# Optimization experiments

Measured on AMD Instinct MI355X. Metric: run time of the kernel, lower is better.

The kernel has to match this reference:

```python
import jax, jax.numpy as jnp
import numpy as np

B, T, IN = 32, 1024, 256
H = 128          # hidden_size
NL = 2           # num_layers
NC = 4           # num_classes
F2 = 2 * H       # bidirectional feature size


def _lstm_dir(xs, w_ih, w_hh, b_ih, b_hh, reverse):
    # xs: [T, B, in]; w_ih: [4H, in]; w_hh: [4H, H]
    if reverse:
        xs = xs[::-1]
    h0 = jnp.zeros((xs.shape[1], H), xs.dtype)
    c0 = jnp.zeros((xs.shape[1], H), xs.dtype)

    def step(carry, xt):
        h, c = carry
        g = xt @ w_ih.T + b_ih + h @ w_hh.T + b_hh  # [B, 4H]
        i, f, gg, o = jnp.split(g, 4, axis=-1)       # PyTorch gate order i,f,g,o
        c = jax.nn.sigmoid(f) * c + jax.nn.sigmoid(i) * jnp.tanh(gg)
        h = jax.nn.sigmoid(o) * jnp.tanh(c)
        return (h, c), h

    _, hs = jax.lax.scan(step, (h0, c0), xs)  # [T, B, H]
    if reverse:
        hs = hs[::-1]
    return hs


def setup_inputs() -> dict:
    key = jax.random.key(0)
    ks = jax.random.split(key, 12)
    s = 0.05
    x = jax.random.normal(ks[0], (B, T, IN), jnp.float32)
    # stacked LSTM params: [layer, direction, ...]; layer0 in = IN, layer1 in = 2H = IN
    w_ih = jax.random.normal(ks[1], (NL, 2, 4 * H, IN), jnp.float32) * s
    w_hh = jax.random.normal(ks[2], (NL, 2, 4 * H, H), jnp.float32) * s
    b_ih = jax.random.normal(ks[3], (NL, 2, 4 * H), jnp.float32) * s
    b_hh = jax.random.normal(ks[4], (NL, 2, 4 * H), jnp.float32) * s
    wq = jax.random.normal(ks[5], (F2, F2), jnp.float32) * s
    wk = jax.random.normal(ks[6], (F2, F2), jnp.float32) * s
    wv = jax.random.normal(ks[7], (F2, F2), jnp.float32) * s
    bq = jax.random.normal(ks[8], (F2,), jnp.float32) * s
    bk = jax.random.normal(ks[9], (F2,), jnp.float32) * s
    bv = jax.random.normal(ks[10], (F2,), jnp.float32) * s
    w_fc = jax.random.normal(ks[11], (NC, F2), jnp.float32) * s
    b_fc = jnp.zeros((NC,), jnp.float32)
    return {"x": x, "w_ih": w_ih, "w_hh": w_hh, "b_ih": b_ih, "b_hh": b_hh,
            "wq": wq, "wk": wk, "wv": wv, "bq": bq, "bk": bk, "bv": bv,
            "w_fc": w_fc, "b_fc": b_fc}


def reference(x, w_ih, w_hh, b_ih, b_hh, wq, wk, wv, bq, bk, bv, w_fc, b_fc):
    # --- biLSTM (eval mode: inter-layer dropout inactive) ---
    xs = jnp.swapaxes(x, 0, 1)  # time-major [T, B, IN]
    for l in range(NL):
        fwd = _lstm_dir(xs, w_ih[l, 0], w_hh[l, 0], b_ih[l, 0], b_hh[l, 0], False)
        bwd = _lstm_dir(xs, w_ih[l, 1], w_hh[l, 1], b_ih[l, 1], b_hh[l, 1], True)
        xs = jnp.concatenate([fwd, bwd], axis=-1)  # [T, B, 2H]
    out = jnp.swapaxes(xs, 0, 1)  # [B, T, 2H]
    # --- naive full self-attention ---
    q = out @ wq.T + bq
    k = out @ wk.T + bk
    v = out @ wv.T + bv
    scores = jnp.einsum('btd,bsd->bts', q, k) / jnp.sqrt(jnp.float32(F2))
    attn = jax.nn.softmax(scores, axis=-1)          # [B, T, T]
    ctx = jnp.einsum('bts,bsd->btd', attn, v)       # [B, T, 2H]
    # --- FC head on last timestep ---
    return ctx[:, -1, :] @ w_fc.T + b_fc            # [B, NC]
```

## Files before the change

kernel.cpp:

```cpp
#include <hip/hip_runtime.h>
#include <math.h>
#include <stdint.h>

#define BB 32
#define TT 1024
#define HH 128
#define G4 512
#define CH 16
#define XPS 516

typedef _Float16 half2_t __attribute__((ext_vector_type(2)));
typedef _Float16 half8_t __attribute__((ext_vector_type(8)));
typedef float f32x4 __attribute__((ext_vector_type(4)));

__device__ __forceinline__ float fdot2f(half2_t a, half2_t b, float c) {
    return __builtin_amdgcn_fdot2(a, b, c, false);
}
__device__ __forceinline__ float rcpf(float x) {
    return __builtin_amdgcn_rcpf(x);
}
__device__ __forceinline__ float dpp_xor1(float x) {
    return __builtin_bit_cast(float, __builtin_amdgcn_update_dpp(
        0, __builtin_bit_cast(int, x), 0xB1, 0xF, 0xF, true));
}
__device__ __forceinline__ float dpp_xor2(float x) {
    return __builtin_bit_cast(float, __builtin_amdgcn_update_dpp(
        0, __builtin_bit_cast(int, x), 0x4E, 0xF, 0xF, true));
}
__device__ __forceinline__ void bar_lgkm() {
    asm volatile("s_waitcnt lgkmcnt(0)\n\ts_barrier" ::: "memory");
}

__global__ __launch_bounds__(256) void cvt_wih(
    const float* __restrict__ w, _Float16* __restrict__ o,
    float* __restrict__ ctxw, float* __restrict__ den, int* __restrict__ cnt)
{
    const int i = (blockIdx.x * 256 + threadIdx.x) * 4;
    float4 f = *(const float4*)(w + i);
    half2_t t[2] = { half2_t{(_Float16)f.x, (_Float16)f.y},
                     half2_t{(_Float16)f.z, (_Float16)f.w} };
    *(float2*)(o + i) = *(float2*)t;
    if (blockIdx.x < 32) ctxw[blockIdx.x * 256 + threadIdx.x] = 0.f;
    if (blockIdx.x == 32 && threadIdx.x < 32) { den[threadIdx.x] = 0.f; cnt[threadIdx.x] = 0; }
}

__global__ __launch_bounds__(512, 1) void lstm_fused(
    const float* __restrict__ x_in,
    const _Float16* __restrict__ wih16_l,
    const float* __restrict__ b_ih_l,
    const float* __restrict__ b_hh_l,
    const float* __restrict__ w_hh_l,
    float* __restrict__ out)
{
    const int b = blockIdx.x & 31;
    const int d = blockIdx.x >> 5;
    const int tid = threadIdx.x;
    const int wvid = tid >> 6;
    const int l = tid & 63;
    const int s = l & 3;
    const int g = l >> 2;
    const int j = (wvid << 4) | g;

    __shared__ __align__(16) _Float16 hs[HH];
    __shared__ __align__(16) float xp[2][CH * XPS];
    __shared__ __align__(16) half2_t xr[2][CH * 128];
    __shared__ __align__(16) float obuf[CH * HH];

    half2_t wv[4][16];
#pragma unroll
    for (int G = 0; G < 4; ++G) {
        const float* wr = w_hh_l + (size_t)(d * G4 + 128 * G + j) * HH + 32 * s;
#pragma unroll
        for (int q4 = 0; q4 < 8; ++q4) {
            float4 f = *(const float4*)(wr + 4 * q4);
            wv[G][2 * q4]     = half2_t{(_Float16)f.x, (_Float16)f.y};
            wv[G][2 * q4 + 1] = half2_t{(_Float16)f.z, (_Float16)f.w};
        }
    }

    const int acol0 = wvid * 64 + (l & 15);
    const _Float16* wn = wih16_l + ((size_t)d * G4 + acol0) * 256 + (l >> 4) * 8;
    const float bias0 = b_ih_l[d * G4 + acol0]      + b_hh_l[d * G4 + acol0];
    const float bias1 = b_ih_l[d * G4 + acol0 + 16] + b_hh_l[d * G4 + acol0 + 16];
    const float bias2 = b_ih_l[d * G4 + acol0 + 32] + b_hh_l[d * G4 + acol0 + 32];
    const float bias3 = b_ih_l[d * G4 + acol0 + 48] + b_hh_l[d * G4 + acol0 + 48];

    const int cbase = ((acol0 & 127) << 2) + (acol0 >> 7);

    const float* xbase = x_in + (size_t)b * TT * 256;

    const int a_noswz = (l & 15) * 512 + (l >> 4) * 16;
    const int a_swz   = (l & 7) << 4;
    const int w_swz_byte = (tid * 16) ^ (((tid >> 5) & 7) << 4);

#pragma unroll 1
    for (int p = 0; p < 2; ++p) {
        const int tlo = d ? (1008 - p * CH) : p * CH;
        const float* gs = xbase + (size_t)tlo * 256 + tid * 8;
        float4 f0 = *(const float4*)gs;
        float4 f1 = *(const float4*)(gs + 4);
        half2_t t4[4] = { half2_t{(_Float16)f0.x, (_Float16)f0.y},
                          half2_t{(_Float16)f0.z, (_Float16)f0.w},
                          half2_t{(_Float16)f1.x, (_Float16)f1.y},
                          half2_t{(_Float16)f1.z, (_Float16)f1.w} };
        *(float4*)((char*)xr[p] + w_swz_byte) = *(float4*)t4;
    }
    __syncthreads();

    f32x4 acc0 = {bias0, bias0, bias0, bias0};
    f32x4 acc1 = {bias1, bias1, bias1, bias1};
    f32x4 acc2 = {bias2, bias2, bias2, bias2};
    f32x4 acc3 = {bias3, bias3, bias3, bias3};

#pragma unroll
    for (int kt = 0; kt < 8; ++kt) {
        half8_t af = *(const half8_t*)((const char*)xr[0] + ((a_noswz + kt * 64) ^ a_swz));
        acc0 = __builtin_amdgcn_mfma_f32_16x16x32_f16(af, *(const half8_t*)(wn +         kt * 32), acc0, 0, 0, 0);
        acc1 = __builtin_amdgcn_mfma_f32_16x16x32_f16(af, *(const half8_t*)(wn +  4096 + kt * 32), acc1, 0, 0, 0);
        acc2 = __builtin_amdgcn_mfma_f32_16x16x32_f16(af, *(const half8_t*)(wn +  8192 + kt * 32), acc2, 0, 0, 0);
        acc3 = __builtin_amdgcn_mfma_f32_16x16x32_f16(af, *(const half8_t*)(wn + 12288 + kt * 32), acc3, 0, 0, 0);
    }
    {
        const int rb = (l >> 4) * 4;
#pragma unroll
        for (int q = 0; q < 4; ++q) {
            const int ix = (rb + q) * XPS + cbase;
            xp[0][ix]       = acc0[q];
            xp[0][ix + 64]  = acc1[q];
            xp[0][ix + 128] = acc2[q];
            xp[0][ix + 192] = acc3[q];
        }
    }
    acc0 = (f32x4){bias0, bias0, bias0, bias0};
    acc1 = (f32x4){bias1, bias1, bias1, bias1};
    acc2 = (f32x4){bias2, bias2, bias2, bias2};
    acc3 = (f32x4){bias3, bias3, bias3, bias3};

    if (tid < 64) ((half2_t*)hs)[tid] = half2_t{(_Float16)0.f, (_Float16)0.f};
    float c = 0.f;
    float* ob = out + (size_t)b * TT * 256 + d * HH;
    __syncthreads();

    float4 rg0 = {}, rg1 = {};
    for (int ck = 0; ck < 64; ++ck) {
        const int cur = ck & 1;
        const bool doproj = (ck + 1 < 64);
        if (ck + 2 < 64) {
            const int tlo2 = d ? (1008 - (ck + 2) * CH) : (ck + 2) * CH;
            const float* gs = xbase + (size_t)tlo2 * 256 + tid * 8;
            rg0 = *(const float4*)gs;
            rg1 = *(const float4*)(gs + 4);
        }
        const float* xb = xp[cur];
        const char* xr_rd = (const char*)xr[cur ^ 1];

        auto rec_step = [&](int si) {
            const int lds_t = d ? (CH - 1 - si) : si;
            const float4 xg4 = *(const float4*)&xb[lds_t * XPS + (j << 2)];

            const float4* hp = (const float4*)(hs + 32 * s);
            float4 hA = hp[0], hB = hp[1], hC = hp[2], hD = hp[3];
            half2_t hh[16];
            hh[0]  = __builtin_bit_cast(half2_t, hA.x);
            hh[1]  = __builtin_bit_cast(half2_t, hA.y);
            hh[2]  = __builtin_bit_cast(half2_t, hA.z);
            hh[3]  = __builtin_bit_cast(half2_t, hA.w);
            hh[4]  = __builtin_bit_cast(half2_t, hB.x);
            hh[5]  = __builtin_bit_cast(half2_t, hB.y);
            hh[6]  = __builtin_bit_cast(half2_t, hB.z);
            hh[7]  = __builtin_bit_cast(half2_t, hB.w);
            hh[8]  = __builtin_bit_cast(half2_t, hC.x);
            hh[9]  = __builtin_bit_cast(half2_t, hC.y);
            hh[10] = __builtin_bit_cast(half2_t, hC.z);
            hh[11] = __builtin_bit_cast(half2_t, hC.w);
            hh[12] = __builtin_bit_cast(half2_t, hD.x);
            hh[13] = __builtin_bit_cast(half2_t, hD.y);
            hh[14] = __builtin_bit_cast(half2_t, hD.z);
            hh[15] = __builtin_bit_cast(half2_t, hD.w);

            float a0 = 0.f, a1 = 0.f, a2 = 0.f, a3 = 0.f;
            float e0 = 0.f, e1 = 0.f, e2 = 0.f, e3 = 0.f;
#pragma unroll
            for (int kk = 0; kk < 8; ++kk) {
                a0 = fdot2f(wv[0][kk], hh[kk], a0);
                a1 = fdot2f(wv[1][kk], hh[kk], a1);
                a2 = fdot2f(wv[2][kk], hh[kk], a2);
                a3 = fdot2f(wv[3][kk], hh[kk], a3);
                e0 = fdot2f(wv[0][kk + 8], hh[kk + 8], e0);
                e1 = fdot2f(wv[1][kk + 8], hh[kk + 8], e1);
                e2 = fdot2f(wv[2][kk + 8], hh[kk + 8], e2);
                e3 = fdot2f(wv[3][kk + 8], hh[kk + 8], e3);
            }
            a0 += e0; a1 += e1; a2 += e2; a3 += e3;

            a0 += dpp_xor1(a0); a0 += dpp_xor2(a0);
            a1 += dpp_xor1(a1); a1 += dpp_xor2(a1);
            a2 += dpp_xor1(a2); a2 += dpp_xor2(a2);
            a3 += dpp_xor1(a3); a3 += dpp_xor2(a3);

            const float gi = rcpf(1.f + __expf(-(a0 + xg4.x)));
            const float gf = rcpf(1.f + __expf(-(a1 + xg4.y)));
            const float gg = 1.f - 2.f * rcpf(1.f + __expf(2.f * (a2 + xg4.z)));
            const float go = rcpf(1.f + __expf(-(a3 + xg4.w)));
            c = gf * c + gi * gg;
            const float th = 1.f - 2.f * rcpf(1.f + __expf(2.f * c));
            const float h = go * th;
            if (s == 0) {
                hs[j] = (_Float16)h;
                obuf[si * HH + j] = h;
            }
        };

        half8_t gbEA = {}, gbEB = {}, gbOA = {}, gbOB = {};
        if (doproj) {
            gbEA = *(const half8_t*)(wn);
            gbEB = *(const half8_t*)(wn + 4096);
        }

#pragma unroll 1
        for (int sp = 0; sp < CH / 2; ++sp) {
            const int kt = sp;
            half8_t afrag = {};
            if (doproj) {
                afrag = *(const half8_t*)(xr_rd + ((a_noswz + kt * 64) ^ a_swz));
                gbOA = *(const half8_t*)(wn +  8192 + kt * 32);
                gbOB = *(const half8_t*)(wn + 12288 + kt * 32);
            }
            rec_step(2 * sp);
            if (doproj) {
                acc0 = __builtin_amdgcn_mfma_f32_16x16x32_f16(afrag, gbEA, acc0, 0, 0, 0);
                acc1 = __builtin_amdgcn_mfma_f32_16x16x32_f16(afrag, gbEB, acc1, 0, 0, 0);
            }
            bar_lgkm();
            if (doproj) {
                const int ktn = (kt + 1) & 7;
                gbEA = *(const half8_t*)(wn +        ktn * 32);
                gbEB = *(const half8_t*)(wn + 4096 + ktn * 32);
            }
            rec_step(2 * sp + 1);
            if (doproj) {
                acc2 = __builtin_amdgcn_mfma_f32_16x16x32_f16(afrag, gbOA, acc2, 0, 0, 0);
                acc3 = __builtin_amdgcn_mfma_f32_16x16x32_f16(afrag, gbOB, acc3, 0, 0, 0);
            }
            bar_lgkm();
        }

        {
            const int idx = tid * 4;
            const int sf = idx >> 7, jf = idx & 127;
            const int sg = ck * CH + sf;
            const int t  = d ? (TT - 1 - sg) : sg;
            float4 o0 = *(const float4*)&obuf[idx];
            *(float4*)&ob[(size_t)t * 256 + jf] = o0;
        }
        if (doproj) {
            float* xpn = xp[cur ^ 1];
            const int rb = (l >> 4) * 4;
#pragma unroll
            for (int q = 0; q < 4; ++q) {
                const int ix = (rb + q) * XPS + cbase;
                xpn[ix]       = acc0[q];
                xpn[ix + 64]  = acc1[q];
                xpn[ix + 128] = acc2[q];
                xpn[ix + 192] = acc3[q];
            }
            acc0 = (f32x4){bias0, bias0, bias0, bias0};
            acc1 = (f32x4){bias1, bias1, bias1, bias1};
            acc2 = (f32x4){bias2, bias2, bias2, bias2};
            acc3 = (f32x4){bias3, bias3, bias3, bias3};
        }
        if (ck + 2 < 64) {
            half2_t t4[4] = { half2_t{(_Float16)rg0.x, (_Float16)rg0.y},
                              half2_t{(_Float16)rg0.z, (_Float16)rg0.w},
                              half2_t{(_Float16)rg1.x, (_Float16)rg1.y},
                              half2_t{(_Float16)rg1.z, (_Float16)rg1.w} };
            *(float4*)((char*)xr[cur] + w_swz_byte) = *(float4*)t4;
        }
        __syncthreads();
    }
}

__global__ __launch_bounds__(256) void attn_all(
    const float* __restrict__ out1,
    const float* __restrict__ wq, const float* __restrict__ bq,
    const float* __restrict__ wk,
    const float* __restrict__ wv, const float* __restrict__ bv,
    const float* __restrict__ wfc, const float* __restrict__ bfc,
    float* __restrict__ ctxw, float* __restrict__ den, int* __restrict__ cnt,
    float* __restrict__ outp)
{
    const int b  = blockIdx.x >> 3;
    const int s8 = blockIdx.x & 7;
    const int tid = threadIdx.x;
    __shared__ float xl[256], q[256];
    __shared__ __align__(16) float r[256];
    __shared__ float ev[128];
    __shared__ float red[256];
    __shared__ int lastflag;

    const float* obase = out1 + (size_t)b * TT * 256;

    xl[tid] = obase[(size_t)(TT - 1) * 256 + tid];
    __syncthreads();
    float acc = bq[tid];
    const float* wqr = wq + (size_t)tid * 256;
#pragma unroll 4
    for (int k = 0; k < 256; ++k) acc += xl[k] * wqr[k];
    q[tid] = acc;
    __syncthreads();
    acc = 0.f;
#pragma unroll 4
    for (int dd = 0; dd < 256; ++dd) acc += q[dd] * wk[(size_t)dd * 256 + tid];
    r[tid] = acc * 0.0625f;
    __syncthreads();

    const float* ob = obase + (size_t)s8 * 128 * 256;
    {
        const int wave = tid >> 6, lane = tid & 63;
        float4 r4 = *(const float4*)&r[lane * 4];
        for (int t = wave; t < 128; t += 4) {
            float4 o4 = *(const float4*)(ob + (size_t)t * 256 + lane * 4);
            float p = r4.x * o4.x + r4.y * o4.y + r4.z * o4.z + r4.w * o4.w;
#pragma unroll
            for (int off = 32; off > 0; off >>= 1) p += __shfl_down(p, off, 64);
            if (lane == 0) ev[t] = expf(p);
        }
    }
    __syncthreads();

    red[tid] = (tid < 128) ? ev[tid] : 0.f;
    __syncthreads();
    for (int st = 128; st > 0; st >>= 1) {
        if (tid < st) red[tid] += red[tid + st];
        __syncthreads();
    }
    if (tid == 0) atomicAdd(&den[b], red[0]);

    acc = 0.f;
#pragma unroll 4
    for (int t = 0; t < 128; ++t) acc += ev[t] * ob[(size_t)t * 256 + tid];
    atomicAdd(&ctxw[b * 256 + tid], acc);

    __syncthreads();
    if (tid == 0) {
        __threadfence();
        const int prev = atomicAdd(&cnt[b], 1);
        lastflag = (prev == 7);
    }
    __syncthreads();
    if (!lastflag) return;

    __threadfence();
    if (tid == 0) red[0] = atomicAdd(&den[b], 0.f);
    const float uu = atomicAdd(&ctxw[b * 256 + tid], 0.f);
    __syncthreads();
    const float inv = 1.f / red[0];
    xl[tid] = uu * inv;
    __syncthreads();

    acc = bv[tid];
    const float* wr = wv + (size_t)tid * 256;
#pragma unroll 4
    for (int k = 0; k < 256; ++k) acc += xl[k] * wr[k];
    q[tid] = acc;
    __syncthreads();

    if (tid < 4) {
        float o = bfc[tid];
        for (int k = 0; k < 256; ++k) o += q[k] * wfc[tid * 256 + k];
        outp[b * 4 + tid] = o;
    }
}

extern "C" void kernel_launch(void* const* d_in, const int* in_sizes, int n_in,
                              void* d_out, int out_size, void* d_ws, size_t ws_size,
                              hipStream_t stream)
{
    const float* x    = (const float*)d_in[0];
    const float* w_ih = (const float*)d_in[1];
    const float* w_hh = (const float*)d_in[2];
    const float* b_ih = (const float*)d_in[3];
    const float* b_hh = (const float*)d_in[4];
    const float* wq   = (const float*)d_in[5];
    const float* wk   = (const float*)d_in[6];
    const float* wv   = (const float*)d_in[7];
    const float* bq   = (const float*)d_in[8];
    const float* bv   = (const float*)d_in[10];
    const float* wfc  = (const float*)d_in[11];
    const float* bfcv = (const float*)d_in[12];
    float* outp = (float*)d_out;

    float* ws = (float*)d_ws;
    _Float16* wih16 = (_Float16*)ws;
    float* out0 = ws + 262144;
    float* out1 = out0 + 8388608;
    float* ctxw = out1 + 8388608;
    float* den  = ctxw + 8192;
    int*   cnt  = (int*)(den + 32);

    cvt_wih<<<512, 256, 0, stream>>>(w_ih, wih16, ctxw, den, cnt);

    lstm_fused<<<64, 512, 0, stream>>>(x, wih16, b_ih, b_hh, w_hh, out0);
    lstm_fused<<<64, 512, 0, stream>>>(out0, wih16 + 262144, b_ih + 1024, b_hh + 1024,
                                       w_hh + 2 * 512 * 128, out1);

    attn_all<<<256, 256, 0, stream>>>(out1, wq, bq, wk, wv, bv, wfc, bfcv,
                                      ctxw, den, cnt, outp);
}
```

Baseline: 1.696 ms.

## Merge both LSTM directions into one 1024-thread block per batch row

Each LSTM launch now runs 32 blocks of 1024 threads, with the forward and backward directions sharing one block per batch element, instead of 64 blocks of 512 threads. The x staging through LDS (the xr buffers, prefetch registers and swizzle) is removed. The input-projection MFMA A fragments are now loaded straight from global memory and converted to fp16 in registers. The change reduces LDS traffic and staging work, but every barrier now synchronises both directions, so the faster direction waits on the slower one each step, and global-load latency sits inside the recurrent loop.

```diff
diff --git a/kernel.cpp b/kernel.cpp
--- a/kernel.cpp
+++ b/kernel.cpp
@@ -44,7 +44,7 @@
     if (blockIdx.x == 32 && threadIdx.x < 32) { den[threadIdx.x] = 0.f; cnt[threadIdx.x] = 0; }
 }
 
-__global__ __launch_bounds__(512, 1) void lstm_fused(
+__global__ __launch_bounds__(1024, 1) void lstm_fused(
     const float* __restrict__ x_in,
     const _Float16* __restrict__ wih16_l,
     const float* __restrict__ b_ih_l,
@@ -52,19 +52,22 @@
     const float* __restrict__ w_hh_l,
     float* __restrict__ out)
 {
-    const int b = blockIdx.x & 31;
-    const int d = blockIdx.x >> 5;
+    const int b = blockIdx.x;
     const int tid = threadIdx.x;
-    const int wvid = tid >> 6;
+    const int d = tid >> 9;
+    const int t5 = tid & 511;
+    const int wvid = t5 >> 6;
     const int l = tid & 63;
     const int s = l & 3;
     const int g = l >> 2;
     const int j = (wvid << 4) | g;
 
-    __shared__ __align__(16) _Float16 hs[HH];
-    __shared__ __align__(16) float xp[2][CH * XPS];
-    __shared__ __align__(16) half2_t xr[2][CH * 128];
-    __shared__ __align__(16) float obuf[CH * HH];
+    __shared__ __align__(16) _Float16 hs[2][HH];
+    __shared__ __align__(16) float xp[2][2][CH * XPS];
+    __shared__ __align__(16) float obuf[2][CH * HH];
+
+    _Float16* hsd = hs[d];
+    float* obufd = obuf[d];
 
     half2_t wv[4][16];
 #pragma unroll
@@ -84,51 +87,43 @@
     const float bias1 = b_ih_l[d * G4 + acol0 + 16] + b_hh_l[d * G4 + acol0 + 16];
     const float bias2 = b_ih_l[d * G4 + acol0 + 32] + b_hh_l[d * G4 + acol0 + 32];
     const float bias3 = b_ih_l[d * G4 + acol0 + 48] + b_hh_l[d * G4 + acol0 + 48];
-
     const int cbase = ((acol0 & 127) << 2) + (acol0 >> 7);
 
     const float* xbase = x_in + (size_t)b * TT * 256;
-
-    const int a_noswz = (l & 15) * 512 + (l >> 4) * 16;
-    const int a_swz   = (l & 7) << 4;
-    const int w_swz_byte = (tid * 16) ^ (((tid >> 5) & 7) << 4);
-
-#pragma unroll 1
-    for (int p = 0; p < 2; ++p) {
-        const int tlo = d ? (1008 - p * CH) : p * CH;
-        const float* gs = xbase + (size_t)tlo * 256 + tid * 8;
-        float4 f0 = *(const float4*)gs;
-        float4 f1 = *(const float4*)(gs + 4);
-        half2_t t4[4] = { half2_t{(_Float16)f0.x, (_Float16)f0.y},
-                          half2_t{(_Float16)f0.z, (_Float16)f0.w},
-                          half2_t{(_Float16)f1.x, (_Float16)f1.y},
-                          half2_t{(_Float16)f1.z, (_Float16)f1.w} };
-        *(float4*)((char*)xr[p] + w_swz_byte) = *(float4*)t4;
-    }
-    __syncthreads();
+    const int arow = l & 15;
+    const int akoff = (l >> 4) * 8;
 
     f32x4 acc0 = {bias0, bias0, bias0, bias0};
     f32x4 acc1 = {bias1, bias1, bias1, bias1};
     f32x4 acc2 = {bias2, bias2, bias2, bias2};
     f32x4 acc3 = {bias3, bias3, bias3, bias3};
 
-#pragma unroll
-    for (int kt = 0; kt < 8; ++kt) {
-        half8_t af = *(const half8_t*)((const char*)xr[0] + ((a_noswz + kt * 64) ^ a_swz));
-        acc0 = __builtin_amdgcn_mfma_f32_16x16x32_f16(af, *(const half8_t*)(wn +         kt * 32), acc0, 0, 0, 0);
-        acc1 = __builtin_amdgcn_mfma_f32_16x16x32_f16(af, *(const half8_t*)(wn +  4096 + kt * 32), acc1, 0, 0, 0);
-        acc2 = __builtin_amdgcn_mfma_f32_16x16x32_f16(af, *(const half8_t*)(wn +  8192 + kt * 32), acc2, 0, 0, 0);
-        acc3 = __builtin_amdgcn_mfma_f32_16x16x32_f16(af, *(const half8_t*)(wn + 12288 + kt * 32), acc3, 0, 0, 0);
-    }
     {
+        const int tlo0 = d ? 1008 : 0;
+        const float* ap = xbase + (size_t)(tlo0 + arow) * 256 + akoff;
+#pragma unroll
+        for (int kt = 0; kt < 8; ++kt) {
+            float4 f0 = *(const float4*)(ap + kt * 32);
+            float4 f1 = *(const float4*)(ap + kt * 32 + 4);
+            half8_t af;
+            af[0] = (_Float16)f0.x; af[1] = (_Float16)f0.y;
+            af[2] = (_Float16)f0.z; af[3] = (_Float16)f0.w;
+            af[4] = (_Float16)f1.x; af[5] = (_Float16)f1.y;
+            af[6] = (_Float16)f1.z; af[7] = (_Float16)f1.w;
+            acc0 = __builtin_amdgcn_mfma_f32_16x16x32_f16(af, *(const half8_t*)(wn +         kt * 32), acc0, 0, 0, 0);
+            acc1 = __builtin_amdgcn_mfma_f32_16x16x32_f16(af, *(const half8_t*)(wn +  4096 + kt * 32), acc1, 0, 0, 0);
+            acc2 = __builtin_amdgcn_mfma_f32_16x16x32_f16(af, *(const half8_t*)(wn +  8192 + kt * 32), acc2, 0, 0, 0);
+            acc3 = __builtin_amdgcn_mfma_f32_16x16x32_f16(af, *(const half8_t*)(wn + 12288 + kt * 32), acc3, 0, 0, 0);
+        }
         const int rb = (l >> 4) * 4;
+        float* xp0 = xp[d][0];
 #pragma unroll
         for (int q = 0; q < 4; ++q) {
             const int ix = (rb + q) * XPS + cbase;
-            xp[0][ix]       = acc0[q];
-            xp[0][ix + 64]  = acc1[q];
-            xp[0][ix + 128] = acc2[q];
-            xp[0][ix + 192] = acc3[q];
+            xp0[ix]       = acc0[q];
+            xp0[ix + 64]  = acc1[q];
+            xp0[ix + 128] = acc2[q];
+            xp0[ix + 192] = acc3[q];
         }
     }
     acc0 = (f32x4){bias0, bias0, bias0, bias0};
@@ -136,29 +131,23 @@
     acc2 = (f32x4){bias2, bias2, bias2, bias2};
     acc3 = (f32x4){bias3, bias3, bias3, bias3};
 
-    if (tid < 64) ((half2_t*)hs)[tid] = half2_t{(_Float16)0.f, (_Float16)0.f};
+    if (t5 < 64) ((half2_t*)hsd)[t5] = half2_t{(_Float16)0.f, (_Float16)0.f};
     float c = 0.f;
     float* ob = out + (size_t)b * TT * 256 + d * HH;
     __syncthreads();
 
-    float4 rg0 = {}, rg1 = {};
     for (int ck = 0; ck < 64; ++ck) {
         const int cur = ck & 1;
         const bool doproj = (ck + 1 < 64);
-        if (ck + 2 < 64) {
-            const int tlo2 = d ? (1008 - (ck + 2) * CH) : (ck + 2) * CH;
-            const float* gs = xbase + (size_t)tlo2 * 256 + tid * 8;
-            rg0 = *(const float4*)gs;
-            rg1 = *(const float4*)(gs + 4);
-        }
-        const float* xb = xp[cur];
-        const char* xr_rd = (const char*)xr[cur ^ 1];
+        const float* xb = xp[d][cur];
+        const int tlo1 = d ? (1008 - (ck + 1) * CH) : (ck + 1) * CH;
+        const float* apn = xbase + (size_t)(tlo1 + arow) * 256 + akoff;
 
         auto rec_step = [&](int si) {
             const int lds_t = d ? (CH - 1 - si) : si;
             const float4 xg4 = *(const float4*)&xb[lds_t * XPS + (j << 2)];
 
-            const float4* hp = (const float4*)(hs + 32 * s);
+            const float4* hp = (const float4*)(hsd + 32 * s);
             float4 hA = hp[0], hB = hp[1], hC = hp[2], hD = hp[3];
             half2_t hh[16];
             hh[0]  = __builtin_bit_cast(half2_t, hA.x);
@@ -206,55 +195,55 @@
             const float th = 1.f - 2.f * rcpf(1.f + __expf(2.f * c));
             const float h = go * th;
             if (s == 0) {
-                hs[j] = (_Float16)h;
-                obuf[si * HH + j] = h;
+                hsd[j] = (_Float16)h;
+                obufd[si * HH + j] = h;
             }
         };
-
-        half8_t gbEA = {}, gbEB = {}, gbOA = {}, gbOB = {};
-        if (doproj) {
-            gbEA = *(const half8_t*)(wn);
-            gbEB = *(const half8_t*)(wn + 4096);
-        }
 
 #pragma unroll 1
         for (int sp = 0; sp < CH / 2; ++sp) {
-            const int kt = sp;
-            half8_t afrag = {};
+            float4 rf0 = {}, rf1 = {};
+            half8_t gbA = {}, gbB = {};
             if (doproj) {
-                afrag = *(const half8_t*)(xr_rd + ((a_noswz + kt * 64) ^ a_swz));
-                gbOA = *(const half8_t*)(wn +  8192 + kt * 32);
-                gbOB = *(const half8_t*)(wn + 12288 + kt * 32);
+                rf0 = *(const float4*)(apn + sp * 32);
+                rf1 = *(const float4*)(apn + sp * 32 + 4);
+                gbA = *(const half8_t*)(wn +        sp * 32);
+                gbB = *(const half8_t*)(wn + 4096 + sp * 32);
             }
             rec_step(2 * sp);
+            half8_t af = {};
             if (doproj) {
-                acc0 = __builtin_amdgcn_mfma_f32_16x16x32_f16(afrag, gbEA, acc0, 0, 0, 0);
-                acc1 = __builtin_amdgcn_mfma_f32_16x16x32_f16(afrag, gbEB, acc1, 0, 0, 0);
+                af[0] = (_Float16)rf0.x; af[1] = (_Float16)rf0.y;
+                af[2] = (_Float16)rf0.z; af[3] = (_Float16)rf0.w;
+                af[4] = (_Float16)rf1.x; af[5] = (_Float16)rf1.y;
+                af[6] = (_Float16)rf1.z; af[7] = (_Float16)rf1.w;
+                acc0 = __builtin_amdgcn_mfma_f32_16x16x32_f16(af, gbA, acc0, 0, 0, 0);
+                acc1 = __builtin_amdgcn_mfma_f32_16x16x32_f16(af, gbB, acc1, 0, 0, 0);
             }
             bar_lgkm();
+            half8_t gbC = {}, gbD = {};
             if (doproj) {
-                const int ktn = (kt + 1) & 7;
-                gbEA = *(const half8_t*)(wn +        ktn * 32);
-                gbEB = *(const half8_t*)(wn + 4096 + ktn * 32);
+                gbC = *(const half8_t*)(wn +  8192 + sp * 32);
+                gbD = *(const half8_t*)(wn + 12288 + sp * 32);
             }
             rec_step(2 * sp + 1);
             if (doproj) {
-                acc2 = __builtin_amdgcn_mfma_f32_16x16x32_f16(afrag, gbOA, acc2, 0, 0, 0);
-                acc3 = __builtin_amdgcn_mfma_f32_16x16x32_f16(afrag, gbOB, acc3, 0, 0, 0);
+                acc2 = __builtin_amdgcn_mfma_f32_16x16x32_f16(af, gbC, acc2, 0, 0, 0);
+                acc3 = __builtin_amdgcn_mfma_f32_16x16x32_f16(af, gbD, acc3, 0, 0, 0);
             }
             bar_lgkm();
         }
 
         {
-            const int idx = tid * 4;
+            const int idx = t5 * 4;
             const int sf = idx >> 7, jf = idx & 127;
             const int sg = ck * CH + sf;
             const int t  = d ? (TT - 1 - sg) : sg;
-            float4 o0 = *(const float4*)&obuf[idx];
+            float4 o0 = *(const float4*)&obufd[idx];
             *(float4*)&ob[(size_t)t * 256 + jf] = o0;
         }
         if (doproj) {
-            float* xpn = xp[cur ^ 1];
+            float* xpn = xp[d][cur ^ 1];
             const int rb = (l >> 4) * 4;
 #pragma unroll
             for (int q = 0; q < 4; ++q) {
@@ -268,13 +257,6 @@
             acc1 = (f32x4){bias1, bias1, bias1, bias1};
             acc2 = (f32x4){bias2, bias2, bias2, bias2};
             acc3 = (f32x4){bias3, bias3, bias3, bias3};
-        }
-        if (ck + 2 < 64) {
-            half2_t t4[4] = { half2_t{(_Float16)rg0.x, (_Float16)rg0.y},
-                              half2_t{(_Float16)rg0.z, (_Float16)rg0.w},
-                              half2_t{(_Float16)rg1.x, (_Float16)rg1.y},
-                              half2_t{(_Float16)rg1.z, (_Float16)rg1.w} };
-            *(float4*)((char*)xr[cur] + w_swz_byte) = *(float4*)t4;
         }
         __syncthreads();
     }
@@ -400,9 +382,9 @@
 
     cvt_wih<<<512, 256, 0, stream>>>(w_ih, wih16, ctxw, den, cnt);
 
-    lstm_fused<<<64, 512, 0, stream>>>(x, wih16, b_ih, b_hh, w_hh, out0);
-    lstm_fused<<<64, 512, 0, stream>>>(out0, wih16 + 262144, b_ih + 1024, b_hh + 1024,
-                                       w_hh + 2 * 512 * 128, out1);
+    lstm_fused<<<32, 1024, 0, stream>>>(x, wih16, b_ih, b_hh, w_hh, out0);
+    lstm_fused<<<32, 1024, 0, stream>>>(out0, wih16 + 262144, b_ih + 1024, b_hh + 1024,
+                                        w_hh + 2 * 512 * 128, out1);
 
     attn_all<<<256, 256, 0, stream>>>(out1, wq, bq, wk, wv, bv, wfc, bfcv,
                                       ctxw, den, cnt, outp);
```

Measured after the change: 4.419 ms. 2.61x slower.
